# Performance work log

Measured on AMD Instinct MI355X. Metric: run time of the kernel, lower is better.

Reference implementation:

```python
import jax, jax.numpy as jnp
import numpy as np
import math

N_EMBD = 1024
N_HEAD = 16
B, T = 2, 2048


def new_gelu(x):
    # GPT-2 tanh-approx GELU (matches torch module exactly)
    return 0.5 * x * (1.0 + jnp.tanh(jnp.sqrt(2.0 / jnp.pi) * (x + 0.044715 * x ** 3)))


def layer_norm(x, w, b, eps=1e-5):
    mu = jnp.mean(x, axis=-1, keepdims=True)
    var = jnp.var(x, axis=-1, keepdims=True)
    return (x - mu) * jax.lax.rsqrt(var + eps) * w + b


def setup_inputs() -> dict:
    key = jax.random.key(0)
    ks = jax.random.split(key, 8)
    C = N_EMBD
    s = 0.02
    return {
        "x": jax.random.normal(ks[0], (B, T, C), dtype=jnp.float32),
        "ln1_w": jnp.ones((C,), jnp.float32),
        "ln1_b": jnp.zeros((C,), jnp.float32),
        "attn_w": s * jax.random.normal(ks[1], (C, 3 * C), jnp.float32),
        "attn_b": jnp.zeros((3 * C,), jnp.float32),
        "attn_proj_w": s * jax.random.normal(ks[2], (C, C), jnp.float32),
        "attn_proj_b": jnp.zeros((C,), jnp.float32),
        "ln2_w": jnp.ones((C,), jnp.float32),
        "ln2_b": jnp.zeros((C,), jnp.float32),
        "fc_w": s * jax.random.normal(ks[3], (C, 4 * C), jnp.float32),
        "fc_b": jnp.zeros((4 * C,), jnp.float32),
        "mlp_proj_w": s * jax.random.normal(ks[4], (4 * C, C), jnp.float32),
        "mlp_proj_b": jnp.zeros((C,), jnp.float32),
    }


def block_forward(x, ln1_w, ln1_b, attn_w, attn_b, attn_proj_w, attn_proj_b,
                  ln2_w, ln2_b, fc_w, fc_b, mlp_proj_w, mlp_proj_b):
    Bm, Tm, C = x.shape
    H = N_HEAD
    D = C // H
    # --- self attention (pre-LN) ---
    h = layer_norm(x, ln1_w, ln1_b)
    qkv = h @ attn_w + attn_b  # [B,T,3C]
    q, k, v = jnp.split(qkv, 3, axis=-1)
    q = q.reshape(Bm, Tm, H, D).transpose(0, 2, 1, 3)  # [B,H,T,D]
    k = k.reshape(Bm, Tm, H, D).transpose(0, 2, 1, 3)
    v = v.reshape(Bm, Tm, H, D).transpose(0, 2, 1, 3)
    att = jnp.einsum('bhqd,bhkd->bhqk', q, k) * (1.0 / math.sqrt(D))
    att = jax.nn.softmax(att, axis=-1)  # NOTE: no causal mask in source
    y = jnp.einsum('bhqk,bhkd->bhqd', att, v)
    y = y.transpose(0, 2, 1, 3).reshape(Bm, Tm, C)
    x = x + (y @ attn_proj_w + attn_proj_b)
    # --- MLP ---
    h = layer_norm(x, ln2_w, ln2_b)
    h = new_gelu(h @ fc_w + fc_b)
    x = x + (h @ mlp_proj_w + mlp_proj_b)
    return x


def reference(x, ln1_w, ln1_b, attn_w, attn_b, attn_proj_w, attn_proj_b,
              ln2_w, ln2_b, fc_w, fc_b, mlp_proj_w, mlp_proj_b):
    return block_forward(x, ln1_w, ln1_b, attn_w, attn_b, attn_proj_w, attn_proj_b,
                         ln2_w, ln2_b, fc_w, fc_b, mlp_proj_w, mlp_proj_b)
```

## Files before the change

kernel.cpp:

```cpp
#include <hip/hip_runtime.h>

typedef __attribute__((ext_vector_type(4)))  float  f32x4;
typedef __attribute__((ext_vector_type(16))) float  f32x16;
typedef __attribute__((ext_vector_type(8)))  short  s16x8;
typedef __attribute__((ext_vector_type(4)))  short  s16x4;
typedef __attribute__((ext_vector_type(4)))  unsigned u32x4;
typedef __attribute__((ext_vector_type(2)))  unsigned u32x2;
typedef __attribute__((ext_vector_type(2)))  int    i32x2;

__device__ __forceinline__ short f2bf(float f) {
    unsigned u = __builtin_bit_cast(unsigned, f);
    u += 0x7fff + ((u >> 16) & 1);
    return (short)(u >> 16);
}

__device__ __forceinline__ void load_lds16(const void* g, void* l) {
    __builtin_amdgcn_global_load_lds(
        (const __attribute__((address_space(1))) unsigned int*)g,
        (__attribute__((address_space(3))) unsigned int*)l, 16, 0, 0);
}

__global__ __launch_bounds__(256) void transpose_cast(const float* __restrict__ W,
                                                      short* __restrict__ Wt,
                                                      int K, int N) {
    __shared__ float t[32][33];
    int n0 = blockIdx.x * 32, k0 = blockIdx.y * 32;
    int tx = threadIdx.x & 31, ty = threadIdx.x >> 5;
#pragma unroll
    for (int i = 0; i < 4; i++)
        t[ty + 8 * i][tx] = W[(size_t)(k0 + ty + 8 * i) * N + n0 + tx];
    __syncthreads();
#pragma unroll
    for (int i = 0; i < 4; i++)
        Wt[(size_t)(n0 + ty + 8 * i) * K + k0 + tx] = f2bf(t[tx][ty + 8 * i]);
}

__global__ __launch_bounds__(256) void vtrans_kernel(const short* __restrict__ qkv,
                                                     short* __restrict__ Vtg) {
    const int T = 2048, C3 = 3072;
    __shared__ short tl[32][33];
    int bh = blockIdx.y >> 1;
    int b = bh >> 4, h = bh & 15;
    int dh = (blockIdx.y & 1) * 32;
    int t0 = blockIdx.x * 32;
    int tx = threadIdx.x & 31, ty = threadIdx.x >> 5;
    const short* src = qkv + (size_t)b * T * C3 + 2048 + h * 64 + dh;
#pragma unroll
    for (int i = 0; i < 4; i++)
        tl[ty + 8 * i][tx] = src[(size_t)(t0 + ty + 8 * i) * C3 + tx];
    __syncthreads();
#pragma unroll
    for (int i = 0; i < 4; i++)
        Vtg[((size_t)bh * 64 + dh + ty + 8 * i) * T + t0 + tx] = tl[tx][ty + 8 * i];
}

__global__ __launch_bounds__(256) void ln_kernel(const float* __restrict__ x,
                                                 const float* __restrict__ w,
                                                 const float* __restrict__ b,
                                                 short* __restrict__ out) {
    int row = blockIdx.x;
    int tid = threadIdx.x;
    const float4 v = ((const float4*)(x + (size_t)row * 1024))[tid];
    float s  = v.x + v.y + v.z + v.w;
    float ss = v.x * v.x + v.y * v.y + v.z * v.z + v.w * v.w;
#pragma unroll
    for (int o = 32; o > 0; o >>= 1) {
        s  += __shfl_down(s, o);
        ss += __shfl_down(ss, o);
    }
    __shared__ float rs[4], rq[4];
    int wave = tid >> 6, lane = tid & 63;
    if (lane == 0) { rs[wave] = s; rq[wave] = ss; }
    __syncthreads();
    float tot = rs[0] + rs[1] + rs[2] + rs[3];
    float tq  = rq[0] + rq[1] + rq[2] + rq[3];
    float mu   = tot * (1.f / 1024.f);
    float var  = tq * (1.f / 1024.f) - mu * mu;
    float rstd = rsqrtf(var + 1e-5f);
    const float4 wv = ((const float4*)w)[tid];
    const float4 bv = ((const float4*)b)[tid];
    s16x4 o;
    o[0] = f2bf((v.x - mu) * rstd * wv.x + bv.x);
    o[1] = f2bf((v.y - mu) * rstd * wv.y + bv.y);
    o[2] = f2bf((v.z - mu) * rstd * wv.z + bv.z);
    o[3] = f2bf((v.w - mu) * rstd * wv.w + bv.w);
    ((s16x4*)(out + (size_t)row * 1024))[tid] = o;
}

template <typename OUT_T, bool GELU, bool RES, bool SCALE_Q>
__global__ __launch_bounds__(256) void gemm_bt(const short* __restrict__ A,
                                               const short* __restrict__ Bt,
                                               const float* __restrict__ bias,
                                               const float* __restrict__ res,
                                               OUT_T* __restrict__ C,
                                               int M, int N, int K) {
    __shared__ __align__(16) short As[128 * 32];
    __shared__ __align__(16) short Bs[128 * 32];
    int tid = threadIdx.x;
    int m0 = blockIdx.y * 128, n0 = blockIdx.x * 128;
    int wave = tid >> 6, lane = tid & 63;
    int wr = wave >> 1, wc = wave & 1;
    int g = lane >> 4, q = lane & 15;
    f32x4 acc[4][4] = {};
    const short* Ab = A + (size_t)m0 * K;
    const short* Bb = Bt + (size_t)n0 * K;
    int srow = tid >> 2;
    int scol = (tid & 3) * 8;
    for (int k0 = 0; k0 < K; k0 += 32) {
        __syncthreads();
        load_lds16(Ab + (size_t)srow * K + k0 + scol, As + tid * 8);
        load_lds16(Ab + (size_t)(srow + 64) * K + k0 + scol, As + 2048 + tid * 8);
        load_lds16(Bb + (size_t)srow * K + k0 + scol, Bs + tid * 8);
        load_lds16(Bb + (size_t)(srow + 64) * K + k0 + scol, Bs + 2048 + tid * 8);
        __syncthreads();
        s16x8 a[4], bf[4];
#pragma unroll
        for (int mi = 0; mi < 4; mi++)
            a[mi] = *(const s16x8*)(As + (wr * 64 + mi * 16 + q) * 32 + g * 8);
#pragma unroll
        for (int ni = 0; ni < 4; ni++)
            bf[ni] = *(const s16x8*)(Bs + (wc * 64 + ni * 16 + q) * 32 + g * 8);
#pragma unroll
        for (int mi = 0; mi < 4; mi++)
#pragma unroll
            for (int ni = 0; ni < 4; ni++)
                acc[mi][ni] = __builtin_amdgcn_mfma_f32_16x16x32_bf16(a[mi], bf[ni], acc[mi][ni], 0, 0, 0);
    }
#pragma unroll
    for (int mi = 0; mi < 4; mi++) {
#pragma unroll
        for (int ni = 0; ni < 4; ni++) {
            int row = m0 + wr * 64 + mi * 16 + g * 4;
            int col = n0 + wc * 64 + ni * 16 + q;
            float bb = bias[col];
#pragma unroll
            for (int r = 0; r < 4; r++) {
                float v = acc[mi][ni][r] + bb;
                if (RES) v += res[(size_t)(row + r) * N + col];
                if (GELU) {
                    float aa = 0.7978845608028654f * (v + 0.044715f * v * v * v);
                    float th = 1.f - 2.f / (__expf(2.f * aa) + 1.f);
                    v = 0.5f * v * (1.f + th);
                }
                if (SCALE_Q && col < 1024) v *= 0.18033688011112042f;
                if constexpr (sizeof(OUT_T) == 2)
                    C[(size_t)(row + r) * N + col] = f2bf(v);
                else
                    C[(size_t)(row + r) * N + col] = v;
            }
        }
    }
}

__global__ __launch_bounds__(256) void gemm_bt_sk(const short* __restrict__ A,
                                                  const short* __restrict__ Bt,
                                                  float* __restrict__ part,
                                                  int M, int N, int K, int Klen) {
    __shared__ __align__(16) short As[128 * 32];
    __shared__ __align__(16) short Bs[128 * 32];
    int tid = threadIdx.x;
    int m0 = blockIdx.y * 128, n0 = blockIdx.x * 128;
    int kz = blockIdx.z;
    int wave = tid >> 6, lane = tid & 63;
    int wr = wave >> 1, wc = wave & 1;
    int g = lane >> 4, q = lane & 15;
    f32x4 acc[4][4] = {};
    const short* Ab = A + (size_t)m0 * K;
    const short* Bb = Bt + (size_t)n0 * K;
    int srow = tid >> 2;
    int scol = (tid & 3) * 8;
    int kend = kz * Klen + Klen;
    for (int k0 = kz * Klen; k0 < kend; k0 += 32) {
        __syncthreads();
        load_lds16(Ab + (size_t)srow * K + k0 + scol, As + tid * 8);
        load_lds16(Ab + (size_t)(srow + 64) * K + k0 + scol, As + 2048 + tid * 8);
        load_lds16(Bb + (size_t)srow * K + k0 + scol, Bs + tid * 8);
        load_lds16(Bb + (size_t)(srow + 64) * K + k0 + scol, Bs + 2048 + tid * 8);
        __syncthreads();
        s16x8 a[4], bf[4];
#pragma unroll
        for (int mi = 0; mi < 4; mi++)
            a[mi] = *(const s16x8*)(As + (wr * 64 + mi * 16 + q) * 32 + g * 8);
#pragma unroll
        for (int ni = 0; ni < 4; ni++)
            bf[ni] = *(const s16x8*)(Bs + (wc * 64 + ni * 16 + q) * 32 + g * 8);
#pragma unroll
        for (int mi = 0; mi < 4; mi++)
#pragma unroll
            for (int ni = 0; ni < 4; ni++)
                acc[mi][ni] = __builtin_amdgcn_mfma_f32_16x16x32_bf16(a[mi], bf[ni], acc[mi][ni], 0, 0, 0);
    }
    float* pb = part + (size_t)kz * M * N;
#pragma unroll
    for (int mi = 0; mi < 4; mi++) {
#pragma unroll
        for (int ni = 0; ni < 4; ni++) {
            int row = m0 + wr * 64 + mi * 16 + g * 4;
            int col = n0 + wc * 64 + ni * 16 + q;
#pragma unroll
            for (int r = 0; r < 4; r++)
                pb[(size_t)(row + r) * N + col] = acc[mi][ni][r];
        }
    }
}

template <int SK>
__global__ __launch_bounds__(256) void reduce_sk(const float* __restrict__ part,
                                                 const float* __restrict__ bias,
                                                 const float* __restrict__ res,
                                                 float* __restrict__ out,
                                                 int MN, int N) {
    int tot = MN >> 2;
    int nb4 = (N >> 2) - 1;
    for (int i = blockIdx.x * 256 + threadIdx.x; i < tot; i += gridDim.x * 256) {
        float4 s = ((const float4*)part)[i];
#pragma unroll
        for (int k = 1; k < SK; k++) {
            float4 p = ((const float4*)(part + (size_t)k * MN))[i];
            s.x += p.x; s.y += p.y; s.z += p.z; s.w += p.w;
        }
        float4 bv = ((const float4*)bias)[i & nb4];
        float4 rv = ((const float4*)res)[i];
        float4 o;
        o.x = s.x + bv.x + rv.x;
        o.y = s.y + bv.y + rv.y;
        o.z = s.z + bv.z + rv.z;
        o.w = s.w + bv.w + rv.w;
        ((float4*)out)[i] = o;
    }
}

__global__ __launch_bounds__(256) void attn_kernel(const short* __restrict__ qkv,
                                                   const short* __restrict__ Vtg,
                                                   short* __restrict__ y) {
    const int T = 2048, C3 = 3072;
    int wg = blockIdx.x;
    int mapped = (wg & 7) * 64 + (wg >> 3);
    int bh = mapped >> 4, qt = mapped & 15;
    int b = bh >> 4, h = bh & 15;
    int tid = threadIdx.x, lane = tid & 63, wave = tid >> 6;
    int ql = lane & 31, hi = lane >> 5;
    const short* base = qkv + (size_t)b * T * C3;

    int qrow = qt * 128 + wave * 32 + ql;
    const short* qp = base + (size_t)qrow * C3 + h * 64;
    s16x8 qf[4];
#pragma unroll
    for (int s = 0; s < 4; s++)
        qf[s] = *(const s16x8*)(qp + ((2 * s + hi) << 3));

    __shared__ __align__(16) short Ks[2][64 * 64];
    __shared__ __align__(16) short Vs[2][64 * 64];

    int srow = tid >> 3, sc8 = tid & 7;
    const short* ksrc = base + 1024 + h * 64 + (size_t)srow * C3 + ((sc8 ^ (srow & 7)) << 3);
    const short* vsrc = Vtg + ((size_t)bh * 64 + srow) * T + ((sc8 ^ (srow & 7)) << 3);

    auto stage = [&](int bi, int t) {
        const short* kp = ksrc + (size_t)(t * 64) * C3;
        load_lds16(kp, &Ks[bi][tid * 8]);
        load_lds16(kp + (size_t)32 * C3, &Ks[bi][tid * 8 + 2048]);
        const short* vp = vsrc + t * 64;
        load_lds16(vp, &Vs[bi][tid * 8]);
        load_lds16(vp + (size_t)32 * T, &Vs[bi][tid * 8 + 2048]);
    };

    float mst = -INFINITY, lst = 0.f;
    f32x16 accY0 = {}, accY1 = {};
    int swz = ql & 7;

    stage(0, 0);
    for (int t = 0; t < 32; ++t) {
        int cur = t & 1;
        __syncthreads();
        if (t < 31) stage(cur ^ 1, t + 1);
        f32x16 s0 = {}, s1 = {};
        const short* kb0 = &Ks[cur][ql * 64];
        const short* kb1 = &Ks[cur][(32 + ql) * 64];
        __builtin_amdgcn_s_setprio(1);
#pragma unroll
        for (int s = 0; s < 4; s++) {
            int c = ((2 * s + hi) ^ swz) << 3;
            s16x8 k0 = *(const s16x8*)(kb0 + c);
            s16x8 k1 = *(const s16x8*)(kb1 + c);
            s0 = __builtin_amdgcn_mfma_f32_32x32x16_bf16(k0, qf[s], s0, 0, 0, 0);
            s1 = __builtin_amdgcn_mfma_f32_32x32x16_bf16(k1, qf[s], s1, 0, 0, 0);
        }
        __builtin_amdgcn_s_setprio(0);
        float tm = fmaxf(s0[0], s0[1]);
#pragma unroll
        for (int r = 2; r < 16; r++) tm = fmaxf(tm, s0[r]);
#pragma unroll
        for (int r = 0; r < 16; r++) tm = fmaxf(tm, s1[r]);
        tm = fmaxf(tm, __shfl_xor(tm, 32));
        if (!__all(tm <= mst + 8.f)) {
            float mnew = fmaxf(mst, tm);
            float alpha = exp2f(mst - mnew);
            lst *= alpha;
#pragma unroll
            for (int r = 0; r < 16; r++) { accY0[r] *= alpha; accY1[r] *= alpha; }
            mst = mnew;
        }
        float ps = 0.f;
#pragma unroll
        for (int r = 0; r < 16; r++) { s0[r] = exp2f(s0[r] - mst); ps += s0[r]; }
#pragma unroll
        for (int r = 0; r < 16; r++) { s1[r] = exp2f(s1[r] - mst); ps += s1[r]; }
        ps += __shfl_xor(ps, 32);
        lst += ps;
        s16x8 pb[4];
#pragma unroll
        for (int s = 0; s < 4; s++) {
            int tt = (s & 1) * 8;
            unsigned lo0, lo1, hi0, hi1;
            if (s < 2) {
                asm("v_cvt_pk_bf16_f32 %0, %1, %2" : "=v"(lo0) : "v"(s0[tt + 0]), "v"(s0[tt + 1]));
                asm("v_cvt_pk_bf16_f32 %0, %1, %2" : "=v"(lo1) : "v"(s0[tt + 2]), "v"(s0[tt + 3]));
                asm("v_cvt_pk_bf16_f32 %0, %1, %2" : "=v"(hi0) : "v"(s0[tt + 4]), "v"(s0[tt + 5]));
                asm("v_cvt_pk_bf16_f32 %0, %1, %2" : "=v"(hi1) : "v"(s0[tt + 6]), "v"(s0[tt + 7]));
            } else {
                asm("v_cvt_pk_bf16_f32 %0, %1, %2" : "=v"(lo0) : "v"(s1[tt + 0]), "v"(s1[tt + 1]));
                asm("v_cvt_pk_bf16_f32 %0, %1, %2" : "=v"(lo1) : "v"(s1[tt + 2]), "v"(s1[tt + 3]));
                asm("v_cvt_pk_bf16_f32 %0, %1, %2" : "=v"(hi0) : "v"(s1[tt + 4]), "v"(s1[tt + 5]));
                asm("v_cvt_pk_bf16_f32 %0, %1, %2" : "=v"(hi1) : "v"(s1[tt + 6]), "v"(s1[tt + 7]));
            }
            i32x2 r0 = __builtin_amdgcn_permlane32_swap((int)hi0, (int)lo0, false, false);
            i32x2 r1 = __builtin_amdgcn_permlane32_swap((int)hi1, (int)lo1, false, false);
            u32x4 w;
            w[0] = (unsigned)r0[1]; w[1] = (unsigned)r1[1];
            w[2] = (unsigned)r0[0]; w[3] = (unsigned)r1[0];
            pb[s] = __builtin_bit_cast(s16x8, w);
        }
        const short* vb0 = &Vs[cur][ql * 64];
        const short* vb1 = &Vs[cur][(32 + ql) * 64];
        __builtin_amdgcn_s_setprio(1);
#pragma unroll
        for (int s = 0; s < 4; s++) {
            int c = ((2 * s + hi) ^ swz) << 3;
            s16x8 v0 = *(const s16x8*)(vb0 + c);
            s16x8 v1 = *(const s16x8*)(vb1 + c);
            accY0 = __builtin_amdgcn_mfma_f32_32x32x16_bf16(v0, pb[s], accY0, 0, 0, 0);
            accY1 = __builtin_amdgcn_mfma_f32_32x32x16_bf16(v1, pb[s], accY1, 0, 0, 0);
        }
        __builtin_amdgcn_s_setprio(0);
    }
    float linv = 1.f / lst;
    short* yrow = y + ((size_t)b * T + qrow) * 1024 + h * 64;
#pragma unroll
    for (int r = 0; r < 4; r++) {
        unsigned w0, w1, w2, w3;
        float a0 = accY0[4 * r] * linv, a1 = accY0[4 * r + 1] * linv;
        float a2 = accY0[4 * r + 2] * linv, a3 = accY0[4 * r + 3] * linv;
        float b0 = accY1[4 * r] * linv, b1 = accY1[4 * r + 1] * linv;
        float b2 = accY1[4 * r + 2] * linv, b3 = accY1[4 * r + 3] * linv;
        asm("v_cvt_pk_bf16_f32 %0, %1, %2" : "=v"(w0) : "v"(a0), "v"(a1));
        asm("v_cvt_pk_bf16_f32 %0, %1, %2" : "=v"(w1) : "v"(a2), "v"(a3));
        asm("v_cvt_pk_bf16_f32 %0, %1, %2" : "=v"(w2) : "v"(b0), "v"(b1));
        asm("v_cvt_pk_bf16_f32 %0, %1, %2" : "=v"(w3) : "v"(b2), "v"(b3));
        u32x2 p0; p0[0] = w0; p0[1] = w1;
        u32x2 p1; p1[0] = w2; p1[1] = w3;
        *(u32x2*)(yrow + 8 * r + 4 * hi)      = p0;
        *(u32x2*)(yrow + 32 + 8 * r + 4 * hi) = p1;
    }
}

extern "C" void kernel_launch(void* const* d_in, const int* in_sizes, int n_in,
                              void* d_out, int out_size, void* d_ws, size_t ws_size,
                              hipStream_t stream) {
    const float* x           = (const float*)d_in[0];
    const float* ln1_w       = (const float*)d_in[1];
    const float* ln1_b       = (const float*)d_in[2];
    const float* attn_w      = (const float*)d_in[3];
    const float* attn_b      = (const float*)d_in[4];
    const float* attn_proj_w = (const float*)d_in[5];
    const float* attn_proj_b = (const float*)d_in[6];
    const float* ln2_w       = (const float*)d_in[7];
    const float* ln2_b       = (const float*)d_in[8];
    const float* fc_w        = (const float*)d_in[9];
    const float* fc_b        = (const float*)d_in[10];
    const float* mlp_proj_w  = (const float*)d_in[11];
    const float* mlp_proj_b  = (const float*)d_in[12];

    const int M = 4096;

    size_t off = 0;
    char* wsb = (char*)d_ws;
    auto alloc = [&](size_t bytes) {
        void* p = wsb + off;
        off += (bytes + 255) & ~(size_t)255;
        return p;
    };
    short* wt_attn  = (short*)alloc(3072ull * 1024 * 2);
    short* wt_proj  = (short*)alloc(1024ull * 1024 * 2);
    short* wt_fc    = (short*)alloc(4096ull * 1024 * 2);
    short* wt_mproj = (short*)alloc(1024ull * 4096 * 2);
    short* h1       = (short*)alloc((size_t)M * 1024 * 2);
    short* qkvb     = (short*)alloc((size_t)M * 3072 * 2);
    short* yb       = (short*)alloc((size_t)M * 1024 * 2);
    float* x1       = (float*)alloc((size_t)M * 1024 * 4);
    short* vtg      = (short*)alloc((size_t)M * 1024 * 2);
    short* h2       = qkvb;

    size_t base_off = off;
    int SK = 0;
    if (ws_size >= base_off + 4ull * M * 1024 * 4) SK = 4;
    else if (ws_size >= base_off + 2ull * M * 1024 * 4) SK = 2;
    float* part = (float*)(wsb + base_off);

    transpose_cast<<<dim3(3072 / 32, 1024 / 32), 256, 0, stream>>>(attn_w, wt_attn, 1024, 3072);
    transpose_cast<<<dim3(1024 / 32, 1024 / 32), 256, 0, stream>>>(attn_proj_w, wt_proj, 1024, 1024);
    transpose_cast<<<dim3(4096 / 32, 1024 / 32), 256, 0, stream>>>(fc_w, wt_fc, 1024, 4096);
    transpose_cast<<<dim3(1024 / 32, 4096 / 32), 256, 0, stream>>>(mlp_proj_w, wt_mproj, 4096, 1024);

    ln_kernel<<<M, 256, 0, stream>>>(x, ln1_w, ln1_b, h1);
    gemm_bt<short, false, false, true><<<dim3(3072 / 128, M / 128), 256, 0, stream>>>(
        h1, wt_attn, attn_b, nullptr, qkvb, M, 3072, 1024);
    vtrans_kernel<<<dim3(2048 / 32, 64), 256, 0, stream>>>(qkvb, vtg);
    attn_kernel<<<512, 256, 0, stream>>>(qkvb, vtg, yb);
    gemm_bt<float, false, true, false><<<dim3(1024 / 128, M / 128), 256, 0, stream>>>(
        yb, wt_proj, attn_proj_b, x, x1, M, 1024, 1024);
    ln_kernel<<<M, 256, 0, stream>>>(x1, ln2_w, ln2_b, h1);
    gemm_bt<short, true, false, false><<<dim3(4096 / 128, M / 128), 256, 0, stream>>>(
        h1, wt_fc, fc_b, nullptr, h2, M, 4096, 1024);

    if (SK == 4) {
        gemm_bt_sk<<<dim3(1024 / 128, M / 128, 4), 256, 0, stream>>>(
            h2, wt_mproj, part, M, 1024, 4096, 1024);
        reduce_sk<4><<<2048, 256, 0, stream>>>(part, mlp_proj_b, x1, (float*)d_out, M * 1024, 1024);
    } else if (SK == 2) {
        gemm_bt_sk<<<dim3(1024 / 128, M / 128, 2), 256, 0, stream>>>(
            h2, wt_mproj, part, M, 1024, 4096, 2048);
        reduce_sk<2><<<2048, 256, 0, stream>>>(part, mlp_proj_b, x1, (float*)d_out, M * 1024, 1024);
    } else {
        gemm_bt<float, false, true, false><<<dim3(1024 / 128, M / 128), 256, 0, stream>>>(
            h2, wt_mproj, mlp_proj_b, x1, (float*)d_out, M, 1024, 4096);
    }
}
```

Before: 308.4 us.

## Remap GEMM tiles per XCD and tree-reduce softmax max/sum in attention

Adds an XCD-aware block remapping to the GEMM and split-K GEMM kernels so that blocks on the same XCD work on adjacent column panels, aiming for better L2 reuse. In the attention kernel, the serial max and sum chains over the 32 score values become tree reductions (3-input fmax and pairwise adds), shortening dependency chains. K/V staging pointers are now advanced incrementally instead of being recomputed each iteration. The remap assumes gridDim.x is divisible by 8, and reordering the sum changes floating-point rounding slightly.

```diff
diff --git a/kernel.cpp b/kernel.cpp
--- a/kernel.cpp
+++ b/kernel.cpp
@@ -18,6 +18,33 @@
     __builtin_amdgcn_global_load_lds(
         (const __attribute__((address_space(1))) unsigned int*)g,
         (__attribute__((address_space(3))) unsigned int*)l, 16, 0, 0);
+}
+
+__device__ __forceinline__ float tmax32(const f32x16& a, const f32x16& b) {
+    float u[11];
+#pragma unroll
+    for (int i = 0; i < 5; i++)
+        u[i] = fmaxf(fmaxf(a[3 * i], a[3 * i + 1]), a[3 * i + 2]);
+    u[5] = fmaxf(a[15], b[0]);
+#pragma unroll
+    for (int i = 0; i < 5; i++)
+        u[6 + i] = fmaxf(fmaxf(b[3 * i + 1], b[3 * i + 2]), b[3 * i + 3]);
+    float v0 = fmaxf(fmaxf(u[0], u[1]), u[2]);
+    float v1 = fmaxf(fmaxf(u[3], u[4]), u[5]);
+    float v2 = fmaxf(fmaxf(u[6], u[7]), u[8]);
+    float v3 = fmaxf(u[9], u[10]);
+    return fmaxf(fmaxf(v0, v1), fmaxf(v2, v3));
+}
+
+__device__ __forceinline__ float tsum32(const f32x16& a, const f32x16& b) {
+    float u[16];
+#pragma unroll
+    for (int i = 0; i < 16; i++) u[i] = a[i] + b[i];
+#pragma unroll
+    for (int i = 0; i < 8; i++) u[i] += u[i + 8];
+#pragma unroll
+    for (int i = 0; i < 4; i++) u[i] += u[i + 4];
+    return (u[0] + u[2]) + (u[1] + u[3]);
 }
 
 __global__ __launch_bounds__(256) void transpose_cast(const float* __restrict__ W,
@@ -87,6 +114,15 @@
     ((s16x4*)(out + (size_t)row * 1024))[tid] = o;
 }
 
+__device__ __forceinline__ void xcd_remap(int& bx, int& by) {
+    int gx = gridDim.x, gy = gridDim.y;
+    int hwid = blockIdx.y * gx + blockIdx.x;
+    int xcd = hwid & 7, rank = hwid >> 3;
+    int pan = gx >> 3;
+    bx = xcd * pan + rank / gy;
+    by = rank % gy;
+}
+
 template <typename OUT_T, bool GELU, bool RES, bool SCALE_Q>
 __global__ __launch_bounds__(256) void gemm_bt(const short* __restrict__ A,
                                                const short* __restrict__ Bt,
@@ -97,7 +133,9 @@
     __shared__ __align__(16) short As[128 * 32];
     __shared__ __align__(16) short Bs[128 * 32];
     int tid = threadIdx.x;
-    int m0 = blockIdx.y * 128, n0 = blockIdx.x * 128;
+    int bx, by;
+    xcd_remap(bx, by);
+    int m0 = by * 128, n0 = bx * 128;
     int wave = tid >> 6, lane = tid & 63;
     int wr = wave >> 1, wc = wave & 1;
     int g = lane >> 4, q = lane & 15;
@@ -159,7 +197,9 @@
     __shared__ __align__(16) short As[128 * 32];
     __shared__ __align__(16) short Bs[128 * 32];
     int tid = threadIdx.x;
-    int m0 = blockIdx.y * 128, n0 = blockIdx.x * 128;
+    int bx, by;
+    xcd_remap(bx, by);
+    int m0 = by * 128, n0 = bx * 128;
     int kz = blockIdx.z;
     int wave = tid >> 6, lane = tid & 63;
     int wr = wave >> 1, wc = wave & 1;
@@ -253,14 +293,12 @@
     __shared__ __align__(16) short Vs[2][64 * 64];
 
     int srow = tid >> 3, sc8 = tid & 7;
-    const short* ksrc = base + 1024 + h * 64 + (size_t)srow * C3 + ((sc8 ^ (srow & 7)) << 3);
-    const short* vsrc = Vtg + ((size_t)bh * 64 + srow) * T + ((sc8 ^ (srow & 7)) << 3);
-
-    auto stage = [&](int bi, int t) {
-        const short* kp = ksrc + (size_t)(t * 64) * C3;
+    const short* kp = base + 1024 + h * 64 + (size_t)srow * C3 + ((sc8 ^ (srow & 7)) << 3);
+    const short* vp = Vtg + ((size_t)bh * 64 + srow) * T + ((sc8 ^ (srow & 7)) << 3);
+
+    auto stage = [&](int bi) {
         load_lds16(kp, &Ks[bi][tid * 8]);
         load_lds16(kp + (size_t)32 * C3, &Ks[bi][tid * 8 + 2048]);
-        const short* vp = vsrc + t * 64;
         load_lds16(vp, &Vs[bi][tid * 8]);
         load_lds16(vp + (size_t)32 * T, &Vs[bi][tid * 8 + 2048]);
     };
@@ -269,11 +307,15 @@
     f32x16 accY0 = {}, accY1 = {};
     int swz = ql & 7;
 
-    stage(0, 0);
+    stage(0);
     for (int t = 0; t < 32; ++t) {
         int cur = t & 1;
         __syncthreads();
-        if (t < 31) stage(cur ^ 1, t + 1);
+        if (t < 31) {
+            kp += 64 * C3;
+            vp += 64;
+            stage(cur ^ 1);
+        }
         f32x16 s0 = {}, s1 = {};
         const short* kb0 = &Ks[cur][ql * 64];
         const short* kb1 = &Ks[cur][(32 + ql) * 64];
@@ -287,11 +329,7 @@
             s1 = __builtin_amdgcn_mfma_f32_32x32x16_bf16(k1, qf[s], s1, 0, 0, 0);
         }
         __builtin_amdgcn_s_setprio(0);
-        float tm = fmaxf(s0[0], s0[1]);
-#pragma unroll
-        for (int r = 2; r < 16; r++) tm = fmaxf(tm, s0[r]);
-#pragma unroll
-        for (int r = 0; r < 16; r++) tm = fmaxf(tm, s1[r]);
+        float tm = tmax32(s0, s1);
         tm = fmaxf(tm, __shfl_xor(tm, 32));
         if (!__all(tm <= mst + 8.f)) {
             float mnew = fmaxf(mst, tm);
@@ -301,11 +339,11 @@
             for (int r = 0; r < 16; r++) { accY0[r] *= alpha; accY1[r] *= alpha; }
             mst = mnew;
         }
-        float ps = 0.f;
-#pragma unroll
-        for (int r = 0; r < 16; r++) { s0[r] = exp2f(s0[r] - mst); ps += s0[r]; }
-#pragma unroll
-        for (int r = 0; r < 16; r++) { s1[r] = exp2f(s1[r] - mst); ps += s1[r]; }
+#pragma unroll
+        for (int r = 0; r < 16; r++) s0[r] = exp2f(s0[r] - mst);
+#pragma unroll
+        for (int r = 0; r < 16; r++) s1[r] = exp2f(s1[r] - mst);
+        float ps = tsum32(s0, s1);
         ps += __shfl_xor(ps, 32);
         lst += ps;
         s16x8 pb[4];
```

Measured after the change: 311.7 us. About the same (+1.1%).
